# Optimization experiments

Hardware: AMD Instinct MI355X
Metric: run time of the kernel (lower is better)

The kernel has to match this reference:

```python
import jax, jax.numpy as jnp
import numpy as np

N = 200_000            # nodes
E = 4_000_000          # edges
GCN_DIMS = [1, 20, 15, 12, 10]
NN_DIMS = [10, 32, 16, 8]
RAW = 16


def setup_inputs() -> dict:
    key = jax.random.key(0)
    ks = jax.random.split(key, 32)
    inp = {
        "x": jax.random.normal(ks[0], (N, GCN_DIMS[0]), dtype=jnp.float32),
        "edge_index": jax.random.randint(ks[1], (2, E), 0, N, dtype=jnp.int64),
    }
    ki = 2
    # GraphConv params: lin_rel (W_rel, b_rel) applied to aggregated neighbors,
    # lin_root (W_root, no bias) applied to self features.
    for i in range(4):
        fi, fo = GCN_DIMS[i], GCN_DIMS[i + 1]
        s = 1.0 / np.sqrt(fi)
        inp[f"gcn{i+1}_Wr"] = jax.random.uniform(ks[ki], (fo, fi), jnp.float32, -s, s); ki += 1
        inp[f"gcn{i+1}_b"]  = jax.random.uniform(ks[ki], (fo,),   jnp.float32, -s, s); ki += 1
        inp[f"gcn{i+1}_Wl"] = jax.random.uniform(ks[ki], (fo, fi), jnp.float32, -s, s); ki += 1
    fc_dims = NN_DIMS + [RAW]
    for i in range(4):
        fi, fo = fc_dims[i], fc_dims[i + 1]
        s = 1.0 / np.sqrt(fi)
        inp[f"fc{i+1}_W"] = jax.random.uniform(ks[ki], (fo, fi), jnp.float32, -s, s); ki += 1
        inp[f"fc{i+1}_b"] = jax.random.uniform(ks[ki], (fo,),   jnp.float32, -s, s); ki += 1
    return inp


def _graph_conv(x, src, tgt, deg_inv, Wr, b, Wl):
    # gather neighbor features, scatter-mean to targets, then two linears
    msg = x[src]                                            # [E, F]
    agg = jax.ops.segment_sum(msg, tgt, num_segments=N)     # [N, F]
    mean = agg * deg_inv                                    # [N, F]
    return mean @ Wr.T + b + x @ Wl.T                       # [N, Fo]


def reference(x, edge_index,
              gcn1_Wr, gcn1_b, gcn1_Wl, gcn2_Wr, gcn2_b, gcn2_Wl,
              gcn3_Wr, gcn3_b, gcn3_Wl, gcn4_Wr, gcn4_b, gcn4_Wl,
              fc1_W, fc1_b, fc2_W, fc2_b, fc3_W, fc3_b, fc4_W, fc4_b):
    sp = jax.nn.softplus
    src, tgt = edge_index[0], edge_index[1]
    cnt = jax.ops.segment_sum(jnp.ones((E,), x.dtype), tgt, num_segments=N)
    deg_inv = (1.0 / jnp.maximum(cnt, 1.0))[:, None]        # mean=0 for isolated nodes
    h = sp(_graph_conv(x, src, tgt, deg_inv, gcn1_Wr, gcn1_b, gcn1_Wl))
    h = sp(_graph_conv(h, src, tgt, deg_inv, gcn2_Wr, gcn2_b, gcn2_Wl))
    h = sp(_graph_conv(h, src, tgt, deg_inv, gcn3_Wr, gcn3_b, gcn3_Wl))
    h = sp(_graph_conv(h, src, tgt, deg_inv, gcn4_Wr, gcn4_b, gcn4_Wl))
    h = sp(h @ fc1_W.T + fc1_b)
    h = sp(h @ fc2_W.T + fc2_b)
    h = sp(h @ fc3_W.T + fc3_b)
    return h @ fc4_W.T + fc4_b
```

## Files before the change

kernel.cpp:

```cpp
#include <hip/hip_runtime.h>
#include <hip/hip_fp16.h>

#define NN 200000
#define NE 4000000

constexpr int BSH = 9;
constexpr int BW = 1 << BSH;
constexpr int NB2 = (NN + BW - 1) / BW;
constexpr int NWG1 = 512;
constexpr int CH = (NE + NWG1 - 1) / NWG1;
constexpr int CAP = 12288;
static_assert(NWG1 == 512, "shifts below assume 512");

__device__ __forceinline__ float softplus_f(float x) {
    return fmaxf(x, 0.0f) + log1pf(expf(-fabsf(x)));
}


__global__ __launch_bounds__(1024) void k_hist(const int* __restrict__ tgt,
                                               int* __restrict__ hist) {
    __shared__ int h[NB2];
    int w = blockIdx.x, t = threadIdx.x;
    for (int i = t; i < NB2; i += 1024) h[i] = 0;
    __syncthreads();
    int lo = w * CH, hi = min(lo + CH, NE);
    for (int e = lo + t; e < hi; e += 1024) atomicAdd(&h[tgt[e] >> BSH], 1);
    __syncthreads();
    for (int i = t; i < NB2; i += 1024) hist[w * NB2 + i] = h[i];
}

__global__ __launch_bounds__(512) void k_colscan(const int* __restrict__ hist,
                                                 int* __restrict__ loc,
                                                 int* __restrict__ bktot) {
    __shared__ int sd[512];
    int b = blockIdx.x, w = threadIdx.x;
    int v = hist[w * NB2 + b];
    sd[w] = v;
    __syncthreads();
    for (int off = 1; off < 512; off <<= 1) {
        int x = (w >= off) ? sd[w - off] : 0;
        __syncthreads();
        sd[w] += x;
        __syncthreads();
    }
    loc[b * NWG1 + w] = sd[w] - v;
    if (w == 511) bktot[b] = sd[511];
}

__global__ __launch_bounds__(512) void k_bktscan(const int* __restrict__ bktot,
                                                 int* __restrict__ bkbase) {
    __shared__ int sd[512];
    int t = threadIdx.x;
    int v = (t < NB2) ? bktot[t] : 0;
    sd[t] = v;
    __syncthreads();
    for (int off = 1; off < 512; off <<= 1) {
        int x = (t >= off) ? sd[t - off] : 0;
        __syncthreads();
        sd[t] += x;
        __syncthreads();
    }
    if (t < NB2) bkbase[t] = sd[t] - v;
    if (t == 0) bkbase[NB2] = NE;
}

__global__ __launch_bounds__(1024) void k_scatter(const int* __restrict__ ei,
                                                  const int* __restrict__ hist,
                                                  const int* __restrict__ loc,
                                                  const int* __restrict__ bkbase,
                                                  unsigned int* __restrict__ pair) {
    __shared__ int h[NB2], lc[NB2], adj[NB2];
    __shared__ int sc[512];
    __shared__ unsigned int stg[CH];
    __shared__ unsigned short stb[CH];
    int w = blockIdx.x, t = threadIdx.x;
    if (t < NB2) h[t] = hist[w * NB2 + t];
    if (t < 512) sc[t] = (t < NB2) ? hist[w * NB2 + t] : 0;
    __syncthreads();
    for (int off = 1; off < 512; off <<= 1) {
        int v = 0;
        if (t < 512 && t >= off) v = sc[t - off];
        __syncthreads();
        if (t < 512) sc[t] += v;
        __syncthreads();
    }
    if (t < NB2) {
        int lbase = sc[t] - h[t];
        lc[t] = lbase;
        adj[t] = loc[t * NWG1 + w] + bkbase[t] - lbase;
    }
    __syncthreads();
    int lo = w * CH, hi = min(lo + CH, NE);
    for (int e = lo + t; e < hi; e += 1024) {
        int s = ei[e], tg = ei[NE + e];
        int b = tg >> BSH;
        int lp = atomicAdd(&lc[b], 1);
        stg[lp] = ((unsigned int)s << BSH) | (unsigned int)(tg & (BW - 1));
        stb[lp] = (unsigned short)b;
    }
    __syncthreads();
    int n = hi - lo;
    for (int i = t; i < n; i += 1024) {
        pair[adj[stb[i]] + i] = stg[i];
    }
}

__global__ __launch_bounds__(1024) void k_bucketfill(const unsigned int* __restrict__ pair,
                                                     const int* __restrict__ bkbase,
                                                     int* __restrict__ rowptr,
                                                     float* __restrict__ dinv,
                                                     int* __restrict__ col) {
    __shared__ int nc[BW], sc[BW], cur[BW];
    __shared__ int colseg[CAP];
    int b = blockIdx.x, t = threadIdx.x;
    int lo = bkbase[b], hi = bkbase[b + 1];
    int cnt = hi - lo;
    if (t < BW) nc[t] = 0;
    __syncthreads();
    for (int e = lo + t; e < hi; e += 1024) atomicAdd(&nc[pair[e] & (BW - 1)], 1);
    __syncthreads();
    if (t < BW) sc[t] = nc[t];
    __syncthreads();
    for (int off = 1; off < BW; off <<= 1) {
        int v = 0;
        if (t < BW && t >= off) v = sc[t - off];
        __syncthreads();
        if (t < BW) sc[t] += v;
        __syncthreads();
    }
    if (t < BW) {
        int nofs = sc[t] - nc[t];
        cur[t] = nofs;
        int g = (b << BSH) + t;
        if (g < NN) {
            rowptr[g] = lo + nofs;
            dinv[g] = 1.0f / fmaxf((float)nc[t], 1.0f);
        }
    }
    if (b == NB2 - 1 && t == 0) rowptr[NN] = NE;
    __syncthreads();
    bool fast = (cnt <= CAP);
    for (int e = lo + t; e < hi; e += 1024) {
        unsigned int v = pair[e];
        int p = atomicAdd(&cur[v & (BW - 1)], 1);
        if (fast) colseg[p] = (int)(v >> BSH);
        else col[lo + p] = (int)(v >> BSH);
    }
    __syncthreads();
    if (fast) {
        for (int i = t; i < cnt; i += 1024) col[lo + i] = colseg[i];
    }
}


union H2U { __half2 h; unsigned int u; };

__device__ __forceinline__ void acc_half8(float* s, uint4 v) {
    H2U a, b, c, d;
    a.u = v.x; b.u = v.y; c.u = v.z; d.u = v.w;
    float2 f;
    f = __half22float2(a.h); s[0] += f.x; s[1] += f.y;
    f = __half22float2(b.h); s[2] += f.x; s[3] += f.y;
    f = __half22float2(c.h); s[4] += f.x; s[5] += f.y;
    f = __half22float2(d.h); s[6] += f.x; s[7] += f.y;
}

__device__ __forceinline__ void store_row16h(__half* p, const float* v) {
    unsigned int ua[8];
#pragma unroll
    for (int i = 0; i < 8; ++i) {
        H2U t;
        t.h = __floats2half2_rn(v[2 * i], v[2 * i + 1]);
        ua[i] = t.u;
    }
    uint4* pu = (uint4*)p;
    pu[0] = make_uint4(ua[0], ua[1], ua[2], ua[3]);
    pu[1] = make_uint4(ua[4], ua[5], ua[6], ua[7]);
}


__global__ __launch_bounds__(512, 6) void k_gcn1(
    const float* __restrict__ x, const int* __restrict__ rowptr,
    const int* __restrict__ col, const float* __restrict__ dinv,
    const float* __restrict__ Wr1, const float* __restrict__ b1,
    const float* __restrict__ Wl1, const float* __restrict__ Wr2,
    const float* __restrict__ b2, const float* __restrict__ Wl2,
    __half* __restrict__ y2, float* __restrict__ z2) {
    __shared__ float sWr1[20], sB1[20], sWl1[20];
    __shared__ float sWr2[15 * 20], sWl2[15 * 20], sB2[15];
    int t = threadIdx.x;
    if (t < 20) { sWr1[t] = Wr1[t]; sB1[t] = b1[t]; sWl1[t] = Wl1[t]; }
    for (int i = t; i < 300; i += 512) { sWr2[i] = Wr2[i]; sWl2[i] = Wl2[i]; }
    if (t < 15) sB2[t] = b2[t];
    __syncthreads();

    int n = blockIdx.x * 256 + (t >> 1);
    int half = t & 1;
    if (n >= NN) return;

    float xn = x[n];
    int beg = rowptr[n], end = rowptr[n + 1];
    float s = 0.f;
    int j = beg + half;
    for (; j + 2 < end; j += 4) {
        int c0 = __ldg(&col[j]), c1 = __ldg(&col[j + 2]);
        s += __ldg(&x[c0]) + __ldg(&x[c1]);
    }
    if (j < end) s += __ldg(&x[__ldg(&col[j])]);
    s += __shfl_xor(s, 1);

    if (half) return;
    float mean = s * dinv[n];
    float h1[20];
#pragma unroll
    for (int o = 0; o < 20; ++o)
        h1[o] = softplus_f(fmaf(mean, sWr1[o], fmaf(xn, sWl1[o], sB1[o])));

    float yo[16], zo[16];
#pragma unroll
    for (int o = 0; o < 15; ++o) {
        float ay = 0.f, az = 0.f;
#pragma unroll
        for (int f = 0; f < 20; ++f) {
            ay = fmaf(h1[f], sWr2[o * 20 + f], ay);
            az = fmaf(h1[f], sWl2[o * 20 + f], az);
        }
        yo[o] = ay;
        zo[o] = az + sB2[o];
    }
    yo[15] = 0.f; zo[15] = 0.f;
    store_row16h(y2 + (size_t)n * 16, yo);
    float4* pz = (float4*)(z2 + (size_t)n * 16);
#pragma unroll
    for (int i = 0; i < 4; ++i)
        pz[i] = make_float4(zo[4 * i], zo[4 * i + 1], zo[4 * i + 2], zo[4 * i + 3]);
}

template <int FO, int NFO>
__global__ __launch_bounds__(512, 6) void k_gcnT(
    const __half* __restrict__ yin, const float* __restrict__ zin,
    const int* __restrict__ rowptr, const int* __restrict__ col,
    const float* __restrict__ dinv, const float* __restrict__ WrN,
    const float* __restrict__ bN, const float* __restrict__ WlN,
    __half* __restrict__ yout, float* __restrict__ zout) {
    __shared__ float sWr[NFO * FO], sWl[NFO * FO], sB[NFO];
    for (int i = threadIdx.x; i < NFO * FO; i += 512) { sWr[i] = WrN[i]; sWl[i] = WlN[i]; }
    if (threadIdx.x < NFO) sB[threadIdx.x] = bN[threadIdx.x];
    __syncthreads();

    int t = threadIdx.x;
    int n = blockIdx.x * 256 + (t >> 1);
    int half = t & 1;
    if (n >= NN) return;

    float s[16];
#pragma unroll
    for (int f = 0; f < 16; ++f) s[f] = 0.f;
    int beg = rowptr[n], end = rowptr[n + 1];
    int j = beg + half;
    for (; j + 2 < end; j += 4) {
        int c0 = __ldg(&col[j]), c1 = __ldg(&col[j + 2]);
        const uint4* p0 = (const uint4*)(yin + (size_t)c0 * 16);
        const uint4* p1 = (const uint4*)(yin + (size_t)c1 * 16);
        uint4 a0 = p0[0], a1 = p0[1], b0 = p1[0], b1 = p1[1];
        acc_half8(s, a0); acc_half8(s + 8, a1);
        acc_half8(s, b0); acc_half8(s + 8, b1);
    }
    if (j < end) {
        const uint4* p0 = (const uint4*)(yin + (size_t)__ldg(&col[j]) * 16);
        uint4 a0 = p0[0], a1 = p0[1];
        acc_half8(s, a0); acc_half8(s + 8, a1);
    }
#pragma unroll
    for (int f = 0; f < 16; ++f) s[f] += __shfl_xor(s[f], 1);

    if (half) return;
    float di = dinv[n];
    const float4* pzr = (const float4*)(zin + (size_t)n * 16);
    float zr[16];
#pragma unroll
    for (int i = 0; i < 4; ++i) {
        float4 v = pzr[i];
        zr[4 * i] = v.x; zr[4 * i + 1] = v.y; zr[4 * i + 2] = v.z; zr[4 * i + 3] = v.w;
    }
    float h[FO];
#pragma unroll
    for (int f = 0; f < FO; ++f) h[f] = softplus_f(fmaf(s[f], di, zr[f]));

    float yo[16], zo[16];
#pragma unroll
    for (int o = 0; o < NFO; ++o) {
        float ay = 0.f, az = 0.f;
#pragma unroll
        for (int f = 0; f < FO; ++f) {
            ay = fmaf(h[f], sWr[o * FO + f], ay);
            az = fmaf(h[f], sWl[o * FO + f], az);
        }
        yo[o] = ay;
        zo[o] = az + sB[o];
    }
#pragma unroll
    for (int o = NFO; o < 16; ++o) { yo[o] = 0.f; zo[o] = 0.f; }
    store_row16h(yout + (size_t)n * 16, yo);
    float4* pz = (float4*)(zout + (size_t)n * 16);
#pragma unroll
    for (int i = 0; i < 4; ++i)
        pz[i] = make_float4(zo[4 * i], zo[4 * i + 1], zo[4 * i + 2], zo[4 * i + 3]);
}

__global__ __launch_bounds__(512, 6) void k_gcn4_fc(
    const __half* __restrict__ yin, const float* __restrict__ zin,
    const int* __restrict__ rowptr, const int* __restrict__ col,
    const float* __restrict__ dinv,
    const float* __restrict__ f1W, const float* __restrict__ f1b,
    const float* __restrict__ f2W, const float* __restrict__ f2b,
    const float* __restrict__ f3W, const float* __restrict__ f3b,
    const float* __restrict__ f4W, const float* __restrict__ f4b,
    float* __restrict__ out) {
    __shared__ float s1W[32 * 10], s1b[32];
    __shared__ float s2W[16 * 32], s2b[16];
    __shared__ float s3W[8 * 16], s3b[8];
    __shared__ float s4W[16 * 8], s4b[16];
    for (int i = threadIdx.x; i < 320; i += 512) s1W[i] = f1W[i];
    for (int i = threadIdx.x; i < 512; i += 512) s2W[i] = f2W[i];
    for (int i = threadIdx.x; i < 128; i += 512) s3W[i] = f3W[i];
    for (int i = threadIdx.x; i < 128; i += 512) s4W[i] = f4W[i];
    if (threadIdx.x < 32) s1b[threadIdx.x] = f1b[threadIdx.x];
    if (threadIdx.x < 16) s2b[threadIdx.x] = f2b[threadIdx.x];
    if (threadIdx.x < 8) s3b[threadIdx.x] = f3b[threadIdx.x];
    if (threadIdx.x < 16) s4b[threadIdx.x] = f4b[threadIdx.x];
    __syncthreads();

    int t = threadIdx.x;
    int n = blockIdx.x * 256 + (t >> 1);
    int half = t & 1;
    if (n >= NN) return;

    float s[16];
#pragma unroll
    for (int f = 0; f < 16; ++f) s[f] = 0.f;
    int beg = rowptr[n], end = rowptr[n + 1];
    int j = beg + half;
    for (; j + 2 < end; j += 4) {
        int c0 = __ldg(&col[j]), c1 = __ldg(&col[j + 2]);
        const uint4* p0 = (const uint4*)(yin + (size_t)c0 * 16);
        const uint4* p1 = (const uint4*)(yin + (size_t)c1 * 16);
        uint4 a0 = p0[0], a1 = p0[1], b0 = p1[0], b1 = p1[1];
        acc_half8(s, a0); acc_half8(s + 8, a1);
        acc_half8(s, b0); acc_half8(s + 8, b1);
    }
    if (j < end) {
        const uint4* p0 = (const uint4*)(yin + (size_t)__ldg(&col[j]) * 16);
        uint4 a0 = p0[0], a1 = p0[1];
        acc_half8(s, a0); acc_half8(s + 8, a1);
    }
#pragma unroll
    for (int f = 0; f < 16; ++f) s[f] += __shfl_xor(s[f], 1);

    if (half) return;
    float di = dinv[n];
    const float4* pzr = (const float4*)(zin + (size_t)n * 16);
    float zr[16];
#pragma unroll
    for (int i = 0; i < 4; ++i) {
        float4 v = pzr[i];
        zr[4 * i] = v.x; zr[4 * i + 1] = v.y; zr[4 * i + 2] = v.z; zr[4 * i + 3] = v.w;
    }
    float a0[10];
#pragma unroll
    for (int f = 0; f < 10; ++f) a0[f] = softplus_f(fmaf(s[f], di, zr[f]));

    float a1[32];
#pragma unroll
    for (int o = 0; o < 32; ++o) {
        float acc = s1b[o];
#pragma unroll
        for (int f = 0; f < 10; ++f) acc = fmaf(a0[f], s1W[o * 10 + f], acc);
        a1[o] = softplus_f(acc);
    }
    float a2[16];
#pragma unroll
    for (int o = 0; o < 16; ++o) {
        float acc = s2b[o];
#pragma unroll
        for (int f = 0; f < 32; ++f) acc = fmaf(a1[f], s2W[o * 32 + f], acc);
        a2[o] = softplus_f(acc);
    }
    float a3[8];
#pragma unroll
    for (int o = 0; o < 8; ++o) {
        float acc = s3b[o];
#pragma unroll
        for (int f = 0; f < 16; ++f) acc = fmaf(a2[f], s3W[o * 16 + f], acc);
        a3[o] = softplus_f(acc);
    }
    float a4[16];
#pragma unroll
    for (int o = 0; o < 16; ++o) {
        float acc = s4b[o];
#pragma unroll
        for (int f = 0; f < 8; ++f) acc = fmaf(a3[f], s4W[o * 8 + f], acc);
        a4[o] = acc;
    }
    float4* po = (float4*)(out + (size_t)n * 16);
#pragma unroll
    for (int i = 0; i < 4; ++i)
        po[i] = make_float4(a4[4 * i], a4[4 * i + 1], a4[4 * i + 2], a4[4 * i + 3]);
}


extern "C" void kernel_launch(void* const* d_in, const int* in_sizes, int n_in,
                              void* d_out, int out_size, void* d_ws, size_t ws_size,
                              hipStream_t stream) {
    const float* x = (const float*)d_in[0];
    const int* ei = (const int*)d_in[1];
    const float* g1Wr = (const float*)d_in[2];
    const float* g1b = (const float*)d_in[3];
    const float* g1Wl = (const float*)d_in[4];
    const float* g2Wr = (const float*)d_in[5];
    const float* g2b = (const float*)d_in[6];
    const float* g2Wl = (const float*)d_in[7];
    const float* g3Wr = (const float*)d_in[8];
    const float* g3b = (const float*)d_in[9];
    const float* g3Wl = (const float*)d_in[10];
    const float* g4Wr = (const float*)d_in[11];
    const float* g4b = (const float*)d_in[12];
    const float* g4Wl = (const float*)d_in[13];
    const float* f1W = (const float*)d_in[14];
    const float* f1b = (const float*)d_in[15];
    const float* f2W = (const float*)d_in[16];
    const float* f2b = (const float*)d_in[17];
    const float* f3W = (const float*)d_in[18];
    const float* f3b = (const float*)d_in[19];
    const float* f4W = (const float*)d_in[20];
    const float* f4b = (const float*)d_in[21];
    float* out = (float*)d_out;

    char* ws = (char*)d_ws;
    size_t off = 0;
    auto alloc = [&](size_t bytes) {
        void* p = ws + off;
        off = (off + bytes + 255) & ~(size_t)255;
        return p;
    };
    int* hist = (int*)alloc((size_t)NWG1 * NB2 * 4);
    int* loc = (int*)alloc((size_t)NB2 * NWG1 * 4);
    int* bktot = (int*)alloc((size_t)NB2 * 4);
    int* bkbase = (int*)alloc((size_t)(NB2 + 1) * 4);
    unsigned int* pair = (unsigned int*)alloc((size_t)NE * 4);
    int* rowptr = (int*)alloc((size_t)(NN + 1) * 4);
    float* dinv = (float*)alloc((size_t)NN * 4);
    int* col = (int*)alloc((size_t)NE * 4);
    float* z2 = (float*)alloc((size_t)NN * 16 * 4);
    __half* y3 = (__half*)alloc((size_t)NN * 16 * 2);
    float* z3 = (float*)alloc((size_t)NN * 16 * 4);
    __half* y2 = (__half*)pair;
    __half* y4 = (__half*)pair;
    float* z4 = z2;

    k_hist<<<NWG1, 1024, 0, stream>>>(ei + NE, hist);
    k_colscan<<<NB2, 512, 0, stream>>>(hist, loc, bktot);
    k_bktscan<<<1, 512, 0, stream>>>(bktot, bkbase);
    k_scatter<<<NWG1, 1024, 0, stream>>>(ei, hist, loc, bkbase, pair);
    k_bucketfill<<<NB2, 1024, 0, stream>>>(pair, bkbase, rowptr, dinv, col);

    const int GB = (NN + 255) / 256;
    k_gcn1<<<GB, 512, 0, stream>>>(x, rowptr, col, dinv, g1Wr, g1b, g1Wl, g2Wr, g2b, g2Wl,
                                   y2, z2);
    k_gcnT<15, 12><<<GB, 512, 0, stream>>>(y2, z2, rowptr, col, dinv, g3Wr, g3b, g3Wl,
                                           y3, z3);
    k_gcnT<12, 10><<<GB, 512, 0, stream>>>(y3, z3, rowptr, col, dinv, g4Wr, g4b, g4Wl,
                                           y4, z4);
    k_gcn4_fc<<<GB, 512, 0, stream>>>(y4, z4, rowptr, col, dinv, f1W, f1b, f2W, f2b, f3W,
                                      f3b, f4W, f4b, out);
}
```

Measured before the change: 600.5 us.

## Split neighbor gather into two source-range passes for cache locality

Each gather-based GCN layer becomes two kernels. The first accumulates only neighbors with index below a split point into a float partial buffer. The second accumulates the remaining neighbors, adds the partial sums and runs the dense epilogue. The aim is to keep each pass's working set of source rows small enough to stay in cache, but the column indices are read twice, a partial buffer is written and read, extra launches are added, and the branches inside the gather loop may diverge.

```diff
diff --git a/kernel.cpp b/kernel.cpp
--- a/kernel.cpp
+++ b/kernel.cpp
@@ -10,6 +10,7 @@
 constexpr int NWG1 = 512;
 constexpr int CH = (NE + NWG1 - 1) / NWG1;
 constexpr int CAP = 12288;
+constexpr int SPLIT = 100000;
 static_assert(NWG1 == 512, "shifts below assume 512");
 
 __device__ __forceinline__ float softplus_f(float x) {
@@ -176,6 +177,39 @@
     uint4* pu = (uint4*)p;
     pu[0] = make_uint4(ua[0], ua[1], ua[2], ua[3]);
     pu[1] = make_uint4(ua[4], ua[5], ua[6], ua[7]);
+}
+
+template <int PASS>
+__device__ __forceinline__ void gather_pass(const __half* __restrict__ yin,
+                                            const int* __restrict__ col,
+                                            int beg, int end, int half, float* s) {
+#pragma unroll
+    for (int f = 0; f < 16; ++f) s[f] = 0.f;
+    int j = beg + half;
+    for (; j + 2 < end; j += 4) {
+        int c0 = __ldg(&col[j]), c1 = __ldg(&col[j + 2]);
+        bool p0 = PASS ? (c0 >= SPLIT) : (c0 < SPLIT);
+        bool p1 = PASS ? (c1 >= SPLIT) : (c1 < SPLIT);
+        if (p0) {
+            const uint4* p = (const uint4*)(yin + (size_t)c0 * 16);
+            uint4 a0 = p[0], a1 = p[1];
+            acc_half8(s, a0); acc_half8(s + 8, a1);
+        }
+        if (p1) {
+            const uint4* p = (const uint4*)(yin + (size_t)c1 * 16);
+            uint4 a0 = p[0], a1 = p[1];
+            acc_half8(s, a0); acc_half8(s + 8, a1);
+        }
+    }
+    if (j < end) {
+        int c = __ldg(&col[j]);
+        bool pr = PASS ? (c >= SPLIT) : (c < SPLIT);
+        if (pr) {
+            const uint4* p = (const uint4*)(yin + (size_t)c * 16);
+            uint4 a0 = p[0], a1 = p[1];
+            acc_half8(s, a0); acc_half8(s + 8, a1);
+        }
+    }
 }
 
 
@@ -236,12 +270,33 @@
         pz[i] = make_float4(zo[4 * i], zo[4 * i + 1], zo[4 * i + 2], zo[4 * i + 3]);
 }
 
+__global__ __launch_bounds__(512, 6) void k_gA(const __half* __restrict__ yin,
+                                               const int* __restrict__ rowptr,
+                                               const int* __restrict__ col,
+                                               float* __restrict__ spart) {
+    int t = threadIdx.x;
+    int n = blockIdx.x * 256 + (t >> 1);
+    int half = t & 1;
+    if (n >= NN) return;
+    int beg = rowptr[n], end = rowptr[n + 1];
+    float s[16];
+    gather_pass<0>(yin, col, beg, end, half, s);
+#pragma unroll
+    for (int f = 0; f < 16; ++f) s[f] += __shfl_xor(s[f], 1);
+    if (half) return;
+    float4* ps = (float4*)(spart + (size_t)n * 16);
+#pragma unroll
+    for (int i = 0; i < 4; ++i)
+        ps[i] = make_float4(s[4 * i], s[4 * i + 1], s[4 * i + 2], s[4 * i + 3]);
+}
+
 template <int FO, int NFO>
-__global__ __launch_bounds__(512, 6) void k_gcnT(
-    const __half* __restrict__ yin, const float* __restrict__ zin,
-    const int* __restrict__ rowptr, const int* __restrict__ col,
-    const float* __restrict__ dinv, const float* __restrict__ WrN,
-    const float* __restrict__ bN, const float* __restrict__ WlN,
+__global__ __launch_bounds__(512, 6) void k_gB_T(
+    const __half* __restrict__ yin, const float* __restrict__ spart,
+    const float* __restrict__ zin, const int* __restrict__ rowptr,
+    const int* __restrict__ col, const float* __restrict__ dinv,
+    const float* __restrict__ WrN, const float* __restrict__ bN,
+    const float* __restrict__ WlN,
     __half* __restrict__ yout, float* __restrict__ zout) {
     __shared__ float sWr[NFO * FO], sWl[NFO * FO], sB[NFO];
     for (int i = threadIdx.x; i < NFO * FO; i += 512) { sWr[i] = WrN[i]; sWl[i] = WlN[i]; }
@@ -252,29 +307,20 @@
     int n = blockIdx.x * 256 + (t >> 1);
     int half = t & 1;
     if (n >= NN) return;
-
+    int beg = rowptr[n], end = rowptr[n + 1];
     float s[16];
-#pragma unroll
-    for (int f = 0; f < 16; ++f) s[f] = 0.f;
-    int beg = rowptr[n], end = rowptr[n + 1];
-    int j = beg + half;
-    for (; j + 2 < end; j += 4) {
-        int c0 = __ldg(&col[j]), c1 = __ldg(&col[j + 2]);
-        const uint4* p0 = (const uint4*)(yin + (size_t)c0 * 16);
-        const uint4* p1 = (const uint4*)(yin + (size_t)c1 * 16);
-        uint4 a0 = p0[0], a1 = p0[1], b0 = p1[0], b1 = p1[1];
-        acc_half8(s, a0); acc_half8(s + 8, a1);
-        acc_half8(s, b0); acc_half8(s + 8, b1);
-    }
-    if (j < end) {
-        const uint4* p0 = (const uint4*)(yin + (size_t)__ldg(&col[j]) * 16);
-        uint4 a0 = p0[0], a1 = p0[1];
-        acc_half8(s, a0); acc_half8(s + 8, a1);
-    }
+    gather_pass<1>(yin, col, beg, end, half, s);
 #pragma unroll
     for (int f = 0; f < 16; ++f) s[f] += __shfl_xor(s[f], 1);
-
     if (half) return;
+
+    const float4* ps = (const float4*)(spart + (size_t)n * 16);
+#pragma unroll
+    for (int i = 0; i < 4; ++i) {
+        float4 v = ps[i];
+        s[4 * i] += v.x; s[4 * i + 1] += v.y; s[4 * i + 2] += v.z; s[4 * i + 3] += v.w;
+    }
+
     float di = dinv[n];
     const float4* pzr = (const float4*)(zin + (size_t)n * 16);
     float zr[16];
@@ -308,10 +354,10 @@
         pz[i] = make_float4(zo[4 * i], zo[4 * i + 1], zo[4 * i + 2], zo[4 * i + 3]);
 }
 
-__global__ __launch_bounds__(512, 6) void k_gcn4_fc(
-    const __half* __restrict__ yin, const float* __restrict__ zin,
-    const int* __restrict__ rowptr, const int* __restrict__ col,
-    const float* __restrict__ dinv,
+__global__ __launch_bounds__(512, 6) void k_gB_fc(
+    const __half* __restrict__ yin, const float* __restrict__ spart,
+    const float* __restrict__ zin, const int* __restrict__ rowptr,
+    const int* __restrict__ col, const float* __restrict__ dinv,
     const float* __restrict__ f1W, const float* __restrict__ f1b,
     const float* __restrict__ f2W, const float* __restrict__ f2b,
     const float* __restrict__ f3W, const float* __restrict__ f3b,
@@ -335,29 +381,20 @@
     int n = blockIdx.x * 256 + (t >> 1);
     int half = t & 1;
     if (n >= NN) return;
-
+    int beg = rowptr[n], end = rowptr[n + 1];
     float s[16];
-#pragma unroll
-    for (int f = 0; f < 16; ++f) s[f] = 0.f;
-    int beg = rowptr[n], end = rowptr[n + 1];
-    int j = beg + half;
-    for (; j + 2 < end; j += 4) {
-        int c0 = __ldg(&col[j]), c1 = __ldg(&col[j + 2]);
-        const uint4* p0 = (const uint4*)(yin + (size_t)c0 * 16);
-        const uint4* p1 = (const uint4*)(yin + (size_t)c1 * 16);
-        uint4 a0 = p0[0], a1 = p0[1], b0 = p1[0], b1 = p1[1];
-        acc_half8(s, a0); acc_half8(s + 8, a1);
-        acc_half8(s, b0); acc_half8(s + 8, b1);
-    }
-    if (j < end) {
-        const uint4* p0 = (const uint4*)(yin + (size_t)__ldg(&col[j]) * 16);
-        uint4 a0 = p0[0], a1 = p0[1];
-        acc_half8(s, a0); acc_half8(s + 8, a1);
-    }
+    gather_pass<1>(yin, col, beg, end, half, s);
 #pragma unroll
     for (int f = 0; f < 16; ++f) s[f] += __shfl_xor(s[f], 1);
-
     if (half) return;
+
+    const float4* ps = (const float4*)(spart + (size_t)n * 16);
+#pragma unroll
+    for (int i = 0; i < 4; ++i) {
+        float4 v = ps[i];
+        s[4 * i] += v.x; s[4 * i + 1] += v.y; s[4 * i + 2] += v.z; s[4 * i + 3] += v.w;
+    }
+
     float di = dinv[n];
     const float4* pzr = (const float4*)(zin + (size_t)n * 16);
     float zr[16];
@@ -454,6 +491,7 @@
     float* z2 = (float*)alloc((size_t)NN * 16 * 4);
     __half* y3 = (__half*)alloc((size_t)NN * 16 * 2);
     float* z3 = (float*)alloc((size_t)NN * 16 * 4);
+    float* spart = (float*)alloc((size_t)NN * 16 * 4);
     __half* y2 = (__half*)pair;
     __half* y4 = (__half*)pair;
     float* z4 = z2;
@@ -467,10 +505,13 @@
     const int GB = (NN + 255) / 256;
     k_gcn1<<<GB, 512, 0, stream>>>(x, rowptr, col, dinv, g1Wr, g1b, g1Wl, g2Wr, g2b, g2Wl,
                                    y2, z2);
-    k_gcnT<15, 12><<<GB, 512, 0, stream>>>(y2, z2, rowptr, col, dinv, g3Wr, g3b, g3Wl,
-                                           y3, z3);
-    k_gcnT<12, 10><<<GB, 512, 0, stream>>>(y3, z3, rowptr, col, dinv, g4Wr, g4b, g4Wl,
-                                           y4, z4);
-    k_gcn4_fc<<<GB, 512, 0, stream>>>(y4, z4, rowptr, col, dinv, f1W, f1b, f2W, f2b, f3W,
-                                      f3b, f4W, f4b, out);
-}
+    k_gA<<<GB, 512, 0, stream>>>(y2, rowptr, col, spart);
+    k_gB_T<15, 12><<<GB, 512, 0, stream>>>(y2, spart, z2, rowptr, col, dinv, g3Wr, g3b,
+                                           g3Wl, y3, z3);
+    k_gA<<<GB, 512, 0, stream>>>(y3, rowptr, col, spart);
+    k_gB_T<12, 10><<<GB, 512, 0, stream>>>(y3, spart, z3, rowptr, col, dinv, g4Wr, g4b,
+                                           g4Wl, y4, z4);
+    k_gA<<<GB, 512, 0, stream>>>(y4, rowptr, col, spart);
+    k_gB_fc<<<GB, 512, 0, stream>>>(y4, spart, z4, rowptr, col, dinv, f1W, f1b, f2W, f2b,
+                                    f3W, f3b, f4W, f4b, out);
+}
```

After: 647.5 us. 7.8% more time.
